# Performance work log

Measured on AMD Instinct MI355X. Metric: run time of the kernel, lower is better.

The kernel has to match this reference:

```python
import jax, jax.numpy as jnp
import numpy as np

EPS = 1e-14

def setup_inputs() -> dict:
    key = jax.random.key(0)
    k1, k2, k3 = jax.random.split(key, 3)
    n = 4096
    batch = 16384
    x = jax.random.normal(k1, (batch, n), dtype=jnp.float32)
    vector = jax.random.normal(k2, (n, 1), dtype=jnp.float32)
    bias = jax.random.normal(k3, (n,), dtype=jnp.float32)
    return {"x": x, "vector": vector, "bias": bias}

def reference(x, vector, bias):
    # normed v: v / (||v|| + eps)
    v = vector[:, 0]  # [n]
    vhat = v / (jnp.sqrt(jnp.sum(v * v)) + EPS)
    # weight = I - 2 vhat vhat^T is symmetric, so x @ W = x - 2 (x @ vhat) vhat^T
    proj = x @ vhat  # [batch]
    out = x - 2.0 * proj[:, None] * vhat[None, :]
    out = out + bias[None, :]
    return out
```

## Files before the change

### kernel.cpp

```cpp
#include <hip/hip_runtime.h>
#include <math.h>


__global__ __launch_bounds__(256) void householder_kernel(
    const float* __restrict__ x,
    const float* __restrict__ v,
    const float* __restrict__ bias,
    float* __restrict__ out,
    int n)
{
    const int row = blockIdx.x;
    const int tid = threadIdx.x;
    const int n4 = n >> 2;
    const float4* __restrict__ xr = (const float4*)(x + (size_t)row * n);
    const float4* __restrict__ vp = (const float4*)v;
    const float4* __restrict__ bp = (const float4*)bias;
    float4* __restrict__ outr = (float4*)(out + (size_t)row * n);

    float4 xreg[4];
    float4 vreg[4];
    float svv = 0.0f;
    float sxv = 0.0f;

    #pragma unroll
    for (int k = 0; k < 4; ++k) {
        const int idx = tid + (k << 8);
        float4 xx = xr[idx];
        float4 vv = vp[idx];
        xreg[k] = xx;
        vreg[k] = vv;
        svv = fmaf(vv.x, vv.x, svv);
        svv = fmaf(vv.y, vv.y, svv);
        svv = fmaf(vv.z, vv.z, svv);
        svv = fmaf(vv.w, vv.w, svv);
        sxv = fmaf(xx.x, vv.x, sxv);
        sxv = fmaf(xx.y, vv.y, sxv);
        sxv = fmaf(xx.z, vv.z, sxv);
        sxv = fmaf(xx.w, vv.w, sxv);
    }

    #pragma unroll
    for (int off = 32; off > 0; off >>= 1) {
        svv += __shfl_down(svv, off, 64);
        sxv += __shfl_down(sxv, off, 64);
    }

    __shared__ float red[8];
    const int wid = tid >> 6;
    if ((tid & 63) == 0) {
        red[wid] = svv;
        red[4 + wid] = sxv;
    }
    __syncthreads();
    svv = red[0] + red[1] + red[2] + red[3];
    sxv = red[4] + red[5] + red[6] + red[7];

    const float inv = 1.0f / (sqrtf(svv) + 1e-14f);
    const float c = 2.0f * inv * inv * sxv;

    #pragma unroll
    for (int k = 0; k < 4; ++k) {
        const int idx = tid + (k << 8);
        const float4 bb = bp[idx];
        const float4 xx = xreg[k];
        const float4 vv = vreg[k];
        float4 o;
        o.x = fmaf(-c, vv.x, xx.x) + bb.x;
        o.y = fmaf(-c, vv.y, xx.y) + bb.y;
        o.z = fmaf(-c, vv.z, xx.z) + bb.z;
        o.w = fmaf(-c, vv.w, xx.w) + bb.w;
        outr[idx] = o;
    }
}

extern "C" void kernel_launch(void* const* d_in, const int* in_sizes, int n_in,
                              void* d_out, int out_size, void* d_ws, size_t ws_size,
                              hipStream_t stream) {
    (void)n_in; (void)d_ws; (void)ws_size;
    const float* x    = (const float*)d_in[0];
    const float* v    = (const float*)d_in[1];
    const float* bias = (const float*)d_in[2];
    float* out = (float*)d_out;

    const int n = in_sizes[1];
    const int batch = in_sizes[0] / n;

    householder_kernel<<<batch, 256, 0, stream>>>(x, v, bias, out, n);
}
```

Measured before the change: 427.8 us.

## Process one row per wavefront with vector staged in shared memory

Each 256-thread block now handles four rows, one per 64-lane wavefront, instead of one row per block. The vector v is loaded once per block into 16 KB of LDS and reused by all four rows. The cross-wave reduction through shared memory and its second barrier are replaced by a wavefront-only xor-shuffle reduction. In exchange each thread holds 16 float4 registers of x, and the LDS footprint plus higher register pressure may reduce occupancy on a kernel that is memory bound.

Result: no change. 432.2 us (+1.0%).

```diff
diff --git a/kernel.cpp b/kernel.cpp
--- a/kernel.cpp
+++ b/kernel.cpp
@@ -9,26 +9,36 @@
     float* __restrict__ out,
     int n)
 {
-    const int row = blockIdx.x;
+    __shared__ float4 vs[1024];
+
     const int tid = threadIdx.x;
-    const int n4 = n >> 2;
-    const float4* __restrict__ xr = (const float4*)(x + (size_t)row * n);
     const float4* __restrict__ vp = (const float4*)v;
-    const float4* __restrict__ bp = (const float4*)bias;
-    float4* __restrict__ outr = (float4*)(out + (size_t)row * n);
 
-    float4 xreg[4];
-    float4 vreg[4];
+    #pragma unroll
+    for (int k = 0; k < 4; ++k) {
+        const int i = tid + (k << 8);
+        vs[i] = vp[i];
+    }
+    __syncthreads();
+
+    const int wid  = tid >> 6;
+    const int lane = tid & 63;
+    const int row  = (blockIdx.x << 2) + wid;
+
+    const float4* __restrict__ xr   = (const float4*)(x + (size_t)row * n);
+    const float4* __restrict__ bp   = (const float4*)bias;
+    float4* __restrict__ outr       = (float4*)(out + (size_t)row * n);
+
+    float4 xreg[16];
     float svv = 0.0f;
     float sxv = 0.0f;
 
     #pragma unroll
-    for (int k = 0; k < 4; ++k) {
-        const int idx = tid + (k << 8);
-        float4 xx = xr[idx];
-        float4 vv = vp[idx];
+    for (int k = 0; k < 16; ++k) {
+        const int idx = lane + (k << 6);
+        const float4 xx = xr[idx];
+        const float4 vv = vs[idx];
         xreg[k] = xx;
-        vreg[k] = vv;
         svv = fmaf(vv.x, vv.x, svv);
         svv = fmaf(vv.y, vv.y, svv);
         svv = fmaf(vv.z, vv.z, svv);
@@ -40,30 +50,20 @@
     }
 
     #pragma unroll
-    for (int off = 32; off > 0; off >>= 1) {
-        svv += __shfl_down(svv, off, 64);
-        sxv += __shfl_down(sxv, off, 64);
+    for (int m = 32; m > 0; m >>= 1) {
+        svv += __shfl_xor(svv, m, 64);
+        sxv += __shfl_xor(sxv, m, 64);
     }
-
-    __shared__ float red[8];
-    const int wid = tid >> 6;
-    if ((tid & 63) == 0) {
-        red[wid] = svv;
-        red[4 + wid] = sxv;
-    }
-    __syncthreads();
-    svv = red[0] + red[1] + red[2] + red[3];
-    sxv = red[4] + red[5] + red[6] + red[7];
 
     const float inv = 1.0f / (sqrtf(svv) + 1e-14f);
     const float c = 2.0f * inv * inv * sxv;
 
     #pragma unroll
-    for (int k = 0; k < 4; ++k) {
-        const int idx = tid + (k << 8);
+    for (int k = 0; k < 16; ++k) {
+        const int idx = lane + (k << 6);
+        const float4 vv = vs[idx];
         const float4 bb = bp[idx];
         const float4 xx = xreg[k];
-        const float4 vv = vreg[k];
         float4 o;
         o.x = fmaf(-c, vv.x, xx.x) + bb.x;
         o.y = fmaf(-c, vv.y, xx.y) + bb.y;
@@ -76,7 +76,7 @@
 extern "C" void kernel_launch(void* const* d_in, const int* in_sizes, int n_in,
                               void* d_out, int out_size, void* d_ws, size_t ws_size,
                               hipStream_t stream) {
-    (void)n_in; (void)d_ws; (void)ws_size;
+    (void)n_in; (void)d_ws; (void)ws_size; (void)out_size;
     const float* x    = (const float*)d_in[0];
     const float* v    = (const float*)d_in[1];
     const float* bias = (const float*)d_in[2];
@@ -84,6 +84,7 @@
 
     const int n = in_sizes[1];
     const int batch = in_sizes[0] / n;
+    const int blocks = batch >> 2;
 
-    householder_kernel<<<batch, 256, 0, stream>>>(x, v, bias, out, n);
+    householder_kernel<<<blocks, 256, 0, stream>>>(x, v, bias, out, n);
 }
```
